# Performance work log

Hardware: AMD Instinct MI355X
Metric: run time of the kernel (lower is better)

Reference implementation:

```python
import jax, jax.numpy as jnp
import numpy as np

H = 64
V = 50257
B = 32
L = 4096
LN_EPS = 1e-5
DELTA_EPS = 1e-6


def setup_inputs() -> dict:
    key = jax.random.key(0)
    ks = jax.random.split(key, 10)
    s = 0.02
    return {
        "seq": jax.random.randint(ks[0], (B, L), 0, V),
        "read_pos": -1,
        "embed": jax.random.normal(ks[1], (V, H), jnp.float32) * s,
        "w1": jax.random.normal(ks[2], (H, 2 * H), jnp.float32) * s,
        "b1": jnp.zeros((2 * H,), jnp.float32),
        "w2": jax.random.normal(ks[3], (2 * H, H), jnp.float32) * s,
        "b2": jnp.zeros((H,), jnp.float32),
        "ln_g": jnp.ones((H,), jnp.float32),
        "ln_b": jnp.zeros((H,), jnp.float32),
        "rp_w": jax.random.normal(ks[4], (H, H), jnp.float32) * s,
        "rp_b": jnp.zeros((H,), jnp.float32),
        "out_w": jax.random.normal(ks[5], (H, V), jnp.float32) * s,
        "out_b": jnp.zeros((V,), jnp.float32),
    }


def _encoder(seq, embed, w1, b1, w2, b2, ln_g, ln_b):
    e = embed[seq]  # [B, L, H]
    f = jnp.maximum(e @ w1 + b1, 0.0) @ w2 + b2  # FFN
    x = e + f
    mu = jnp.mean(x, axis=-1, keepdims=True)
    var = jnp.mean((x - mu) ** 2, axis=-1, keepdims=True)
    return (x - mu) * jax.lax.rsqrt(var + LN_EPS) * ln_g + ln_b


def _delta_memory(h_all):
    # Strictly sequential delta-rule fast-weight update over t = 0..L-2.
    Bs, Ls, Hs = h_all.shape
    keys = jnp.transpose(h_all[:, : Ls - 1, :], (1, 0, 2))  # [L-1, B, H]

    def step(M, k):
        vp = jnp.einsum('bij,bj->bi', M, k)  # M @ k
        u = k - vp / (jnp.sum(k * k, axis=-1, keepdims=True) + DELTA_EPS)
        M = M + u[:, :, None] * k[:, None, :]  # outer product update
        return M, None

    M0 = jnp.zeros((Bs, Hs, Hs), h_all.dtype)
    M, _ = jax.lax.scan(step, M0, keys)
    return M


def reference(seq, read_pos, embed, w1, b1, w2, b2, ln_g, ln_b, rp_w, rp_b, out_w, out_b):
    h_all = _encoder(seq, embed, w1, b1, w2, b2, ln_g, ln_b)  # [B, L, H]
    M = _delta_memory(h_all)  # [B, H, H]
    q = h_all[:, read_pos, :]  # [B, H]
    r = jnp.einsum('bij,bj->bi', M, q)
    return (r @ rp_w + rp_b) @ out_w + out_b  # [B, V]
```

## Files before the change

kernel.cpp:

```cpp
#include <hip/hip_runtime.h>

#define HH 64
#define VV 50257
#define BB 32
#define LL 4096

constexpr float LN_EPS_F = 1e-5f;
constexpr float DELTA_EPS_F = 1e-6f;

constexpr int CS = 64;
constexpr int NG = LL / CS;

typedef float f32x4 __attribute__((ext_vector_type(4)));
typedef short bf16x8 __attribute__((ext_vector_type(8)));
union U16x8 { uint4 u; bf16x8 v; unsigned short s[8]; };

__device__ __forceinline__ unsigned short f2bf(float f) {
  union { float f; unsigned u; } v; v.f = f;
  unsigned r = v.u + 0x7fff + ((v.u >> 16) & 1);
  return (unsigned short)(r >> 16);
}

template <int CTRL>
__device__ __forceinline__ float dpp_add(float x) {
  int t = __builtin_amdgcn_update_dpp(0, __float_as_int(x), CTRL, 0xF, 0xF, true);
  return x + __int_as_float(t);
}

__device__ __forceinline__ float wave_sum_lane63(float x) {
  x = dpp_add<0x111>(x);
  x = dpp_add<0x112>(x);
  x = dpp_add<0x114>(x);
  x = dpp_add<0x118>(x);
  x = dpp_add<0x142>(x);
  x = dpp_add<0x143>(x);
  return x;
}

__device__ __forceinline__ float readlane_f(float x, int lane) {
  return __int_as_float(__builtin_amdgcn_readlane(__float_as_int(x), lane));
}

__global__ __launch_bounds__(256) void prep_kernel(
    const float* __restrict__ w1, const float* __restrict__ w2,
    unsigned short* __restrict__ w1b, unsigned short* __restrict__ w2b) {
  int i = blockIdx.x * 256 + threadIdx.x;
  if (i < 8192) {
    int jj = i >> 6, h = i & 63;
    w1b[i] = f2bf(w1[h * 128 + jj]);
  } else {
    int k = i - 8192;
    int h = k >> 7, jj = k & 127;
    w2b[k] = f2bf(w2[jj * 64 + h]);
  }
}

__global__ __launch_bounds__(64, 1) void encoder_kernel(
    const int* __restrict__ seq, const float* __restrict__ embed,
    const unsigned short* __restrict__ w1b, const float* __restrict__ b1,
    const unsigned short* __restrict__ w2b, const float* __restrict__ b2,
    const float* __restrict__ ln_g, const float* __restrict__ ln_b,
    float* __restrict__ h_all, float* __restrict__ beta) {
  __shared__ __align__(16) char pool[26624];
  unsigned short (*e_l)[72] = reinterpret_cast<unsigned short (*)[72]>(pool);
  unsigned short (*act_l)[136] = reinterpret_cast<unsigned short (*)[136]>(pool + 9216);
  float (*x_l)[65] = reinterpret_cast<float (*)[65]>(pool);
  __shared__ float2 gb_l[64];
  __shared__ float b1_l[128], b2_l[64];

  int lane = threadIdx.x;
  int q = lane >> 4, l = lane & 15;
  int base = blockIdx.x * 64;
  int s = seq[base + lane];

  {
    const float4* ep = reinterpret_cast<const float4*>(embed + (size_t)s * HH);
#pragma unroll
    for (int i = 0; i < 8; ++i) {
      float4 va = ep[2 * i], vb = ep[2 * i + 1];
      uint4 u;
      u.x = (unsigned)f2bf(va.x) | ((unsigned)f2bf(va.y) << 16);
      u.y = (unsigned)f2bf(va.z) | ((unsigned)f2bf(va.w) << 16);
      u.z = (unsigned)f2bf(vb.x) | ((unsigned)f2bf(vb.y) << 16);
      u.w = (unsigned)f2bf(vb.z) | ((unsigned)f2bf(vb.w) << 16);
      *(uint4*)&e_l[lane][8 * i] = u;
    }
  }
  gb_l[lane] = make_float2(ln_g[lane], ln_b[lane]);
  b1_l[lane] = b1[lane];
  b1_l[64 + lane] = b1[64 + lane];
  b2_l[lane] = b2[lane];

  bf16x8 af1[8][2];
#pragma unroll
  for (int mi = 0; mi < 8; ++mi)
#pragma unroll
    for (int ks = 0; ks < 2; ++ks) {
      U16x8 t;
      t.u = *(const uint4*)(w1b + (mi * 16 + l) * 64 + ks * 32 + q * 8);
      af1[mi][ks] = t.v;
    }

  __syncthreads();

  f32x4 acc1[8][4];
#pragma unroll
  for (int mi = 0; mi < 8; ++mi)
#pragma unroll
    for (int nt = 0; nt < 4; ++nt) acc1[mi][nt] = (f32x4){0.f, 0.f, 0.f, 0.f};

#pragma unroll
  for (int ks = 0; ks < 2; ++ks) {
    bf16x8 bfr[4];
#pragma unroll
    for (int nt = 0; nt < 4; ++nt) {
      U16x8 t;
      t.u = *(const uint4*)&e_l[nt * 16 + l][ks * 32 + q * 8];
      bfr[nt] = t.v;
    }
#pragma unroll
    for (int mi = 0; mi < 8; ++mi)
#pragma unroll
      for (int nt = 0; nt < 4; ++nt)
        acc1[mi][nt] = __builtin_amdgcn_mfma_f32_16x16x32_bf16(
            af1[mi][ks], bfr[nt], acc1[mi][nt], 0, 0, 0);
  }

#pragma unroll
  for (int mi = 0; mi < 8; ++mi)
#pragma unroll
    for (int nt = 0; nt < 4; ++nt) {
      int tok = nt * 16 + l;
      int jj0 = mi * 16 + q * 4;
      float v0 = fmaxf(acc1[mi][nt][0] + b1_l[jj0 + 0], 0.f);
      float v1 = fmaxf(acc1[mi][nt][1] + b1_l[jj0 + 1], 0.f);
      float v2 = fmaxf(acc1[mi][nt][2] + b1_l[jj0 + 2], 0.f);
      float v3 = fmaxf(acc1[mi][nt][3] + b1_l[jj0 + 3], 0.f);
      uint2 u;
      u.x = (unsigned)f2bf(v0) | ((unsigned)f2bf(v1) << 16);
      u.y = (unsigned)f2bf(v2) | ((unsigned)f2bf(v3) << 16);
      *(uint2*)&act_l[tok][jj0] = u;
    }

  bf16x8 bf2[4][4];
#pragma unroll
  for (int nt = 0; nt < 4; ++nt)
#pragma unroll
    for (int ks = 0; ks < 4; ++ks) {
      U16x8 t;
      t.u = *(const uint4*)(w2b + (nt * 16 + l) * 128 + ks * 32 + q * 8);
      bf2[nt][ks] = t.v;
    }

  __syncthreads();

  f32x4 acc2[4][4];
#pragma unroll
  for (int mt = 0; mt < 4; ++mt)
#pragma unroll
    for (int nt = 0; nt < 4; ++nt) acc2[mt][nt] = (f32x4){0.f, 0.f, 0.f, 0.f};

#pragma unroll
  for (int ks = 0; ks < 4; ++ks) {
    bf16x8 afr[4];
#pragma unroll
    for (int mt = 0; mt < 4; ++mt) {
      U16x8 t;
      t.u = *(const uint4*)&act_l[mt * 16 + l][ks * 32 + q * 8];
      afr[mt] = t.v;
    }
#pragma unroll
    for (int mt = 0; mt < 4; ++mt)
#pragma unroll
      for (int nt = 0; nt < 4; ++nt)
        acc2[mt][nt] = __builtin_amdgcn_mfma_f32_16x16x32_bf16(
            afr[mt], bf2[nt][ks], acc2[mt][nt], 0, 0, 0);
  }

  __syncthreads();

#pragma unroll
  for (int mt = 0; mt < 4; ++mt)
#pragma unroll
    for (int nt = 0; nt < 4; ++nt) {
      int h = nt * 16 + l;
#pragma unroll
      for (int r = 0; r < 4; ++r) {
        int tok = mt * 16 + q * 4 + r;
        x_l[tok][h] = acc2[mt][nt][r] + b2_l[h];
      }
    }

  __syncthreads();

  float x[HH];
#pragma unroll
  for (int h = 0; h < HH; ++h) x[h] = x_l[lane][h];
  {
    const float4* ep = reinterpret_cast<const float4*>(embed + (size_t)s * HH);
#pragma unroll
    for (int i = 0; i < 16; ++i) {
      float4 v = ep[i];
      x[4 * i + 0] += v.x; x[4 * i + 1] += v.y;
      x[4 * i + 2] += v.z; x[4 * i + 3] += v.w;
    }
  }
  float sum = 0.f;
#pragma unroll
  for (int h = 0; h < HH; ++h) sum += x[h];
  float mu = sum * (1.f / HH);
  float vs = 0.f;
#pragma unroll
  for (int h = 0; h < HH; ++h) { float dx = x[h] - mu; vs = fmaf(dx, dx, vs); }
  float rstd = rsqrtf(vs * (1.f / HH) + LN_EPS_F);

  float ss = 0.f;
#pragma unroll
  for (int h = 0; h < HH; ++h) {
    float2 gb = gb_l[h];
    float o = fmaf((x[h] - mu) * rstd, gb.x, gb.y);
    ss = fmaf(o, o, ss);
    x[h] = o;
  }
  float4* hp = reinterpret_cast<float4*>(h_all + (size_t)(base + lane) * HH);
#pragma unroll
  for (int i = 0; i < 16; ++i)
    hp[i] = make_float4(x[4 * i + 0], x[4 * i + 1], x[4 * i + 2], x[4 * i + 3]);
  beta[base + lane] = 1.f / (ss + DELTA_EPS_F);
}

__global__ __launch_bounds__(64, 1) void gram_n_kernel(
    const float* __restrict__ h_all, const float* __restrict__ beta,
    float* __restrict__ Ng) {
  __shared__ __align__(16) char smem[37120];
  unsigned short (*pA)[64][72] = reinterpret_cast<unsigned short (*)[64][72]>(smem);
  unsigned short (*pB)[64][72] = reinterpret_cast<unsigned short (*)[64][72]>(smem + 18432);
  float* Glp = reinterpret_cast<float*>(smem + 18432);
  float* bl = reinterpret_cast<float*>(smem + 36864);

  int c = blockIdx.x, b = blockIdx.y, lane = threadIdx.x;
  int q = lane >> 4, l = lane & 15;
  const float* src = h_all + ((size_t)b * LL + c * CS) * HH;

  bf16x8 ah[2][4], al_[2][4];
#pragma unroll
  for (int ks = 0; ks < 2; ++ks)
#pragma unroll
    for (int i = 0; i < 4; ++i) {
      const float* p = src + (i * 16 + l) * 64 + ks * 32 + q * 8;
      float4 va = *(const float4*)p, vb = *(const float4*)(p + 4);
      float f[8] = {va.x, va.y, va.z, va.w, vb.x, vb.y, vb.z, vb.w};
      U16x8 hi, lo;
#pragma unroll
      for (int r = 0; r < 8; ++r) {
        unsigned short hb = f2bf(f[r]);
        hi.s[r] = hb;
        lo.s[r] = f2bf(f[r] - __uint_as_float(((unsigned)hb) << 16));
      }
      ah[ks][i] = hi.v; al_[ks][i] = lo.v;
    }
  if (c == NG - 1 && l == 15) {
#pragma unroll
    for (int ks = 0; ks < 2; ++ks) {
      ah[ks][3] = (bf16x8){0, 0, 0, 0, 0, 0, 0, 0};
      al_[ks][3] = (bf16x8){0, 0, 0, 0, 0, 0, 0, 0};
    }
  }

  bl[lane] = beta[(size_t)b * LL + c * CS + lane];

  float m[64];
#pragma unroll
  for (int t = 0; t < 64; ++t) m[t] = src[t * 64 + lane];
  if (c == NG - 1) m[63] = 0.f;

  f32x4 acc[4][4];
#pragma unroll
  for (int mi = 0; mi < 4; ++mi)
#pragma unroll
    for (int nt = 0; nt <= mi; ++nt) acc[mi][nt] = (f32x4){0.f, 0.f, 0.f, 0.f};

#pragma unroll
  for (int ks = 0; ks < 2; ++ks)
#pragma unroll
    for (int mi = 0; mi < 4; ++mi)
#pragma unroll
      for (int nt = 0; nt <= mi; ++nt) {
        acc[mi][nt] = __builtin_amdgcn_mfma_f32_16x16x32_bf16(ah[ks][mi], ah[ks][nt], acc[mi][nt], 0, 0, 0);
        acc[mi][nt] = __builtin_amdgcn_mfma_f32_16x16x32_bf16(ah[ks][mi], al_[ks][nt], acc[mi][nt], 0, 0, 0);
        acc[mi][nt] = __builtin_amdgcn_mfma_f32_16x16x32_bf16(al_[ks][mi], ah[ks][nt], acc[mi][nt], 0, 0, 0);
      }

#pragma unroll
  for (int mi = 0; mi < 4; ++mi) {
    int gg = 4 * mi + q;
    int e1 = 8 * gg * (gg + 1);
    int o0 = 4 * gg * (2 * gg + 1);
    int o1 = e1;
    int o2 = e1 + 4 * (gg + 1);
    int o3 = e1 + 8 * (gg + 1);
#pragma unroll
    for (int nt = 0; nt < mi; ++nt) {
      int t = nt * 16 + l;
      Glp[o0 + t] = acc[mi][nt][0];
      Glp[o1 + t] = acc[mi][nt][1];
      Glp[o2 + t] = acc[mi][nt][2];
      Glp[o3 + t] = acc[mi][nt][3];
    }
    {
      int t = mi * 16 + l;
      if (l < 4 * q)     Glp[o0 + t] = acc[mi][mi][0];
      if (l < 4 * q + 1) Glp[o1 + t] = acc[mi][mi][1];
      if (l < 4 * q + 2) Glp[o2 + t] = acc[mi][mi][2];
      if (l < 4 * q + 3) Glp[o3 + t] = acc[mi][mi][3];
    }
  }

#pragma unroll
  for (int i = 0; i < 16; ++i) {
    float v0 = m[4 * i], v1 = m[4 * i + 1], v2 = m[4 * i + 2], v3 = m[4 * i + 3];
    unsigned short h0 = f2bf(v0), h1 = f2bf(v1), h2 = f2bf(v2), h3 = f2bf(v3);
    float r0 = v0 - __uint_as_float(((unsigned)h0) << 16);
    float r1 = v1 - __uint_as_float(((unsigned)h1) << 16);
    float r2 = v2 - __uint_as_float(((unsigned)h2) << 16);
    float r3 = v3 - __uint_as_float(((unsigned)h3) << 16);
    *(uint2*)&pA[0][lane][4 * i] = make_uint2(
        (unsigned)h0 | (((unsigned)h1) << 16), (unsigned)h2 | (((unsigned)h3) << 16));
    *(uint2*)&pA[1][lane][4 * i] = make_uint2(
        (unsigned)f2bf(r0) | (((unsigned)f2bf(r1)) << 16),
        (unsigned)f2bf(r2) | (((unsigned)f2bf(r3)) << 16));
  }
  __syncthreads();

#pragma unroll
  for (int g = 15; g >= 0; --g) {
    int e1 = 8 * g * (g + 1);
    int o0 = 4 * g * (2 * g + 1);
    int o1 = e1;
    int o2 = e1 + 4 * (g + 1);
    int o3 = e1 + 8 * (g + 1);
    float4 C1 = *(const float4*)(Glp + o1 + 4 * g);
    float4 C2 = *(const float4*)(Glp + o2 + 4 * g);
    float4 C3 = *(const float4*)(Glp + o3 + 4 * g);
    float4 B4 = *(const float4*)(bl + 4 * g);

    float t3 = B4.w * m[4 * g + 3];
    float v2 = fmaf(-C3.z, t3, m[4 * g + 2]);
    float t2 = B4.z * v2;
    float v1 = fmaf(-C2.y, t2, fmaf(-C3.y, t3, m[4 * g + 1]));
    float t1 = B4.y * v1;
    float v0 = fmaf(-C1.x, t1, fmaf(-C2.x, t2, fmaf(-C3.x, t3, m[4 * g + 0])));
    float t0 = B4.x * v0;
    m[4 * g + 0] = t0; m[4 * g + 1] = t1; m[4 * g + 2] = t2; m[4 * g + 3] = t3;

#pragma unroll
    for (int j = 0; j < g; ++j) {
      float4 R0 = *(const float4*)(Glp + o0 + 4 * j);
      float4 R1 = *(const float4*)(Glp + o1 + 4 * j);
      float4 R2 = *(const float4*)(Glp + o2 + 4 * j);
      float4 R3 = *(const float4*)(Glp + o3 + 4 * j);
      m[4 * j + 0] = fmaf(-R3.x, t3, fmaf(-R2.x, t2, fmaf(-R1.x, t1, fmaf(-R0.x, t0, m[4 * j + 0]))));
      m[4 * j + 1] = fmaf(-R3.y, t3, fmaf(-R2.y, t2, fmaf(-R1.y, t1, fmaf(-R0.y, t0, m[4 * j + 1]))));
      m[4 * j + 2] = fmaf(-R3.z, t3, fmaf(-R2.z, t2, fmaf(-R1.z, t1, fmaf(-R0.z, t0, m[4 * j + 2]))));
      m[4 * j + 3] = fmaf(-R3.w, t3, fmaf(-R2.w, t2, fmaf(-R1.w, t1, fmaf(-R0.w, t0, m[4 * j + 3]))));
    }
  }

  __syncthreads();

#pragma unroll
  for (int i = 0; i < 16; ++i) {
    float v0 = m[4 * i], v1 = m[4 * i + 1], v2 = m[4 * i + 2], v3 = m[4 * i + 3];
    unsigned short h0 = f2bf(v0), h1 = f2bf(v1), h2 = f2bf(v2), h3 = f2bf(v3);
    float r0 = v0 - __uint_as_float(((unsigned)h0) << 16);
    float r1 = v1 - __uint_as_float(((unsigned)h1) << 16);
    float r2 = v2 - __uint_as_float(((unsigned)h2) << 16);
    float r3 = v3 - __uint_as_float(((unsigned)h3) << 16);
    *(uint2*)&pB[0][lane][4 * i] = make_uint2(
        (unsigned)h0 | (((unsigned)h1) << 16), (unsigned)h2 | (((unsigned)h3) << 16));
    *(uint2*)&pB[1][lane][4 * i] = make_uint2(
        (unsigned)f2bf(r0) | (((unsigned)f2bf(r1)) << 16),
        (unsigned)f2bf(r2) | (((unsigned)f2bf(r3)) << 16));
  }
  __syncthreads();

  f32x4 acc2[4][4];
#pragma unroll
  for (int mi = 0; mi < 4; ++mi)
#pragma unroll
    for (int nt = 0; nt < 4; ++nt) acc2[mi][nt] = (f32x4){0.f, 0.f, 0.f, 0.f};

#pragma unroll
  for (int ks = 0; ks < 2; ++ks) {
    bf16x8 kh[4], kl_[4], bh[4], blo[4];
#pragma unroll
    for (int i = 0; i < 4; ++i) {
      U16x8 t;
      t.u = *(const uint4*)&pA[0][i * 16 + l][ks * 32 + q * 8]; kh[i] = t.v;
      t.u = *(const uint4*)&pA[1][i * 16 + l][ks * 32 + q * 8]; kl_[i] = t.v;
      t.u = *(const uint4*)&pB[0][i * 16 + l][ks * 32 + q * 8]; bh[i] = t.v;
      t.u = *(const uint4*)&pB[1][i * 16 + l][ks * 32 + q * 8]; blo[i] = t.v;
    }
#pragma unroll
    for (int mi = 0; mi < 4; ++mi)
#pragma unroll
      for (int nt = 0; nt < 4; ++nt) {
        acc2[mi][nt] = __builtin_amdgcn_mfma_f32_16x16x32_bf16(kh[mi], bh[nt], acc2[mi][nt], 0, 0, 0);
        acc2[mi][nt] = __builtin_amdgcn_mfma_f32_16x16x32_bf16(kh[mi], blo[nt], acc2[mi][nt], 0, 0, 0);
        acc2[mi][nt] = __builtin_amdgcn_mfma_f32_16x16x32_bf16(kl_[mi], bh[nt], acc2[mi][nt], 0, 0, 0);
      }
  }

  float* np = Ng + (((size_t)b * NG + c) << 12);
#pragma unroll
  for (int mi = 0; mi < 4; ++mi)
#pragma unroll
    for (int nt = 0; nt < 4; ++nt) {
      int h0 = mi * 16 + q * 4, hp = nt * 16 + l;
      float4 v;
      v.x = ((h0 + 0 == hp) ? 1.f : 0.f) - acc2[mi][nt][0];
      v.y = ((h0 + 1 == hp) ? 1.f : 0.f) - acc2[mi][nt][1];
      v.z = ((h0 + 2 == hp) ? 1.f : 0.f) - acc2[mi][nt][2];
      v.w = ((h0 + 3 == hp) ? 1.f : 0.f) - acc2[mi][nt][3];
      *(float4*)&np[hp * 64 + h0] = v;
    }
}

__global__ __launch_bounds__(64, 1) void boundary_kernel(
    const float* __restrict__ h_all, const float* __restrict__ Ng,
    const int* __restrict__ read_pos_p, float* __restrict__ Qg) {
  __shared__ __align__(16) float nt0[64 * 64];
  __shared__ __align__(16) float nt1[64 * 64];
  __shared__ __align__(16) float ql[64];

  int b = blockIdx.x, lane = threadIdx.x;
  int rpv = read_pos_p[0];
  int pos = rpv < 0 ? rpv + LL : rpv;
  float Q = h_all[((size_t)b * LL + pos) * HH + lane];

  const float* Nb = Ng + ((size_t)b * NG << 12);

  auto load_chunk = [&](float* buf, int c) {
    const float* g = Nb + ((size_t)c << 12);
#pragma unroll
    for (int i = 0; i < 16; ++i)
      __builtin_amdgcn_global_load_lds(
          (const __attribute__((address_space(1))) unsigned*)(g + i * 256 + lane * 4),
          (__attribute__((address_space(3))) unsigned*)(buf + i * 256), 16, 0, 0);
  };

  auto step = [&](const float* buf, int c, bool last) {
    if (last) __builtin_amdgcn_s_waitcnt(0x0F70);
    else      __builtin_amdgcn_s_waitcnt(0x4F70);
    Qg[((size_t)b * NG + c) * HH + lane] = Q;
    ql[lane] = Q;
    float a0 = 0.f, a1 = 0.f, a2 = 0.f, a3 = 0.f;
#pragma unroll
    for (int j = 0; j < 64; j += 4) {
      float4 q4 = *(const float4*)&ql[j];
      a0 = fmaf(buf[(j + 0) * 64 + lane], q4.x, a0);
      a1 = fmaf(buf[(j + 1) * 64 + lane], q4.y, a1);
      a2 = fmaf(buf[(j + 2) * 64 + lane], q4.z, a2);
      a3 = fmaf(buf[(j + 3) * 64 + lane], q4.w, a3);
    }
    Q = (a0 + a1) + (a2 + a3);
  };

  load_chunk(nt1, NG - 1);
  load_chunk(nt0, NG - 2);

#pragma unroll 1
  for (int c = NG - 1; c >= 1; c -= 2) {
    step(nt1, c, false);
    __builtin_amdgcn_s_waitcnt(0xC07F);
    if (c >= 3) load_chunk(nt1, c - 2);
    step(nt0, c - 1, c == 1);
    __builtin_amdgcn_s_waitcnt(0xC07F);
    if (c >= 3) load_chunk(nt0, c - 3);
  }
}

__global__ __launch_bounds__(64, 1) void chunk_scan_kernel(
    const float* __restrict__ h_all, const float* __restrict__ beta,
    const float* __restrict__ Qg, float* __restrict__ rc) {
  int c = blockIdx.x, b = blockIdx.y, j = threadIdx.x;
  const float* hb = h_all + (size_t)b * LL * HH;
  const float* betab = beta + (size_t)b * LL;

  float P = Qg[((size_t)b * NG + c) * HH + j];
  float r = 0.f;

  float kk[CS];
#pragma unroll
  for (int i = 0; i < CS; ++i) kk[i] = hb[((size_t)(c * CS + i)) * HH + j];
  float bv = betab[c * CS + j];

  bool last = (c == NG - 1);
#pragma unroll
  for (int i = CS - 1; i >= 0; --i) {
    float k = kk[i];
    float bt = readlane_f(bv, i);
    float m = k * P;
    float s = wave_sum_lane63(m);
    float d = readlane_f(s, 63);
    if (i == CS - 1 && last) d = 0.f;
    r = fmaf(d, k, r);
    P = fmaf(-(bt * d), k, P);
  }
  rc[((size_t)b * NG + c) * HH + j] = r;
}

__global__ __launch_bounds__(64, 1) void combine_kernel(
    const float* __restrict__ rc, const float* __restrict__ rp_w,
    const float* __restrict__ rp_b, float* __restrict__ yv) {
  int b = blockIdx.x, j = threadIdx.x;
  float r = 0.f;
#pragma unroll 8
  for (int cc = 0; cc < NG; ++cc) r += rc[((size_t)b * NG + cc) * HH + j];
  __shared__ float rs[HH];
  rs[j] = r;
  __syncthreads();
  float yj = rp_b[j];
#pragma unroll
  for (int h = 0; h < HH; ++h) yj = fmaf(rs[h], rp_w[h * HH + j], yj);
  yv[b * HH + j] = yj;
}

__global__ __launch_bounds__(256, 2) void out_kernel(
    const float* __restrict__ yv, const float* __restrict__ out_w,
    const float* __restrict__ out_b, float* __restrict__ out) {
  __shared__ float ys[BB * HH];
  for (int i = threadIdx.x; i < BB * HH; i += 256) ys[i] = yv[i];
  __syncthreads();

  int v = blockIdx.x * 256 + threadIdx.x;
  if (v >= VV) return;

  float acc[BB];
  float ob = out_b[v];
#pragma unroll
  for (int b = 0; b < BB; ++b) acc[b] = ob;

  for (int h = 0; h < HH; ++h) {
    float w = out_w[(size_t)h * VV + v];
#pragma unroll
    for (int b = 0; b < BB; ++b) acc[b] = fmaf(ys[b * HH + h], w, acc[b]);
  }
#pragma unroll
  for (int b = 0; b < BB; ++b) out[(size_t)b * VV + v] = acc[b];
}

extern "C" void kernel_launch(void* const* d_in, const int* in_sizes, int n_in,
                              void* d_out, int out_size, void* d_ws, size_t ws_size,
                              hipStream_t stream) {
  (void)in_sizes; (void)n_in; (void)out_size; (void)ws_size;
  const int*   seq   = (const int*)d_in[0];
  const int*   rp    = (const int*)d_in[1];
  const float* embed = (const float*)d_in[2];
  const float* w1    = (const float*)d_in[3];
  const float* b1    = (const float*)d_in[4];
  const float* w2    = (const float*)d_in[5];
  const float* b2    = (const float*)d_in[6];
  const float* ln_g  = (const float*)d_in[7];
  const float* ln_b  = (const float*)d_in[8];
  const float* rp_w  = (const float*)d_in[9];
  const float* rp_b  = (const float*)d_in[10];
  const float* out_w = (const float*)d_in[11];
  const float* out_b = (const float*)d_in[12];
  float* out = (float*)d_out;

  float* h_all = (float*)d_ws;
  float* beta  = h_all + (size_t)BB * LL * HH;
  float* Ng    = beta + (size_t)BB * LL;
  float* Qg    = Ng + (size_t)BB * NG * HH * HH;
  float* rcv   = Qg + (size_t)BB * NG * HH;
  float* yv    = rcv + (size_t)BB * NG * HH;
  unsigned short* w1b = (unsigned short*)(yv + (size_t)BB * HH);
  unsigned short* w2b = w1b + 8192;

  prep_kernel<<<64, 256, 0, stream>>>(w1, w2, w1b, w2b);
  encoder_kernel<<<BB * LL / 64, 64, 0, stream>>>(seq, embed, w1b, b1, w2b, b2,
                                                  ln_g, ln_b, h_all, beta);
  gram_n_kernel<<<dim3(NG, BB), 64, 0, stream>>>(h_all, beta, Ng);
  boundary_kernel<<<BB, 64, 0, stream>>>(h_all, Ng, rp, Qg);
  chunk_scan_kernel<<<dim3(NG, BB), 64, 0, stream>>>(h_all, beta, Qg, rcv);
  combine_kernel<<<BB, 64, 0, stream>>>(rcv, rp_w, rp_b, yv);
  out_kernel<<<(VV + 255) / 256, 256, 0, stream>>>(yv, out_w, out_b, out);
}
```

Before: 232.1 us.

## Use packed bf16 conversion, packed FMA solve, and half-staged swizzled LDS

Replaces the software bf16 rounding with the hardware v_cvt_pk_bf16_f32 instruction in the encoder and the gram kernel. The triangular-solve state becomes float2 vectors so the inner updates can use packed FMA. The pB staging buffer is cut to two XOR-swizzled half buffers that are filled per k-step, which shrinks the gram kernel's LDS from about 37KB to about 27KB and avoids bank conflicts. The cost is extra __syncthreads inside the k loop, and the hardware conversion's rounding may differ slightly from the manual round-to-nearest-even.

After: 235.3 us. Within noise of the previous version (+1.4%).

```diff
diff --git a/kernel.cpp b/kernel.cpp
--- a/kernel.cpp
+++ b/kernel.cpp
@@ -12,6 +12,7 @@
 constexpr int NG = LL / CS;
 
 typedef float f32x4 __attribute__((ext_vector_type(4)));
+typedef float f32x2 __attribute__((ext_vector_type(2)));
 typedef short bf16x8 __attribute__((ext_vector_type(8)));
 union U16x8 { uint4 u; bf16x8 v; unsigned short s[8]; };
 
@@ -19,6 +20,19 @@
   union { float f; unsigned u; } v; v.f = f;
   unsigned r = v.u + 0x7fff + ((v.u >> 16) & 1);
   return (unsigned short)(r >> 16);
+}
+
+__device__ __forceinline__ unsigned cvt_pk_bf16(float a, float b) {
+  unsigned r;
+  asm("v_cvt_pk_bf16_f32 %0, %1, %2" : "=v"(r) : "v"(a), "v"(b));
+  return r;
+}
+
+__device__ __forceinline__ void split2(float a, float b, unsigned& hp, unsigned& lp) {
+  hp = cvt_pk_bf16(a, b);
+  float ha = __uint_as_float(hp << 16);
+  float hb = __uint_as_float(hp & 0xffff0000u);
+  lp = cvt_pk_bf16(a - ha, b - hb);
 }
 
 template <int CTRL>
@@ -79,10 +93,10 @@
     for (int i = 0; i < 8; ++i) {
       float4 va = ep[2 * i], vb = ep[2 * i + 1];
       uint4 u;
-      u.x = (unsigned)f2bf(va.x) | ((unsigned)f2bf(va.y) << 16);
-      u.y = (unsigned)f2bf(va.z) | ((unsigned)f2bf(va.w) << 16);
-      u.z = (unsigned)f2bf(vb.x) | ((unsigned)f2bf(vb.y) << 16);
-      u.w = (unsigned)f2bf(vb.z) | ((unsigned)f2bf(vb.w) << 16);
+      u.x = cvt_pk_bf16(va.x, va.y);
+      u.y = cvt_pk_bf16(va.z, va.w);
+      u.z = cvt_pk_bf16(vb.x, vb.y);
+      u.w = cvt_pk_bf16(vb.z, vb.w);
       *(uint4*)&e_l[lane][8 * i] = u;
     }
   }
@@ -137,8 +151,8 @@
       float v2 = fmaxf(acc1[mi][nt][2] + b1_l[jj0 + 2], 0.f);
       float v3 = fmaxf(acc1[mi][nt][3] + b1_l[jj0 + 3], 0.f);
       uint2 u;
-      u.x = (unsigned)f2bf(v0) | ((unsigned)f2bf(v1) << 16);
-      u.y = (unsigned)f2bf(v2) | ((unsigned)f2bf(v3) << 16);
+      u.x = cvt_pk_bf16(v0, v1);
+      u.y = cvt_pk_bf16(v2, v3);
       *(uint2*)&act_l[tok][jj0] = u;
     }
 
@@ -232,11 +246,11 @@
 __global__ __launch_bounds__(64, 1) void gram_n_kernel(
     const float* __restrict__ h_all, const float* __restrict__ beta,
     float* __restrict__ Ng) {
-  __shared__ __align__(16) char smem[37120];
+  __shared__ __align__(16) char smem[27136];
   unsigned short (*pA)[64][72] = reinterpret_cast<unsigned short (*)[64][72]>(smem);
-  unsigned short (*pB)[64][72] = reinterpret_cast<unsigned short (*)[64][72]>(smem + 18432);
   float* Glp = reinterpret_cast<float*>(smem + 18432);
-  float* bl = reinterpret_cast<float*>(smem + 36864);
+  char* pBh0 = smem + 18432;
+  float* bl = reinterpret_cast<float*>(smem + 26880);
 
   int c = blockIdx.x, b = blockIdx.y, lane = threadIdx.x;
   int q = lane >> 4, l = lane & 15;
@@ -249,14 +263,11 @@
     for (int i = 0; i < 4; ++i) {
       const float* p = src + (i * 16 + l) * 64 + ks * 32 + q * 8;
       float4 va = *(const float4*)p, vb = *(const float4*)(p + 4);
-      float f[8] = {va.x, va.y, va.z, va.w, vb.x, vb.y, vb.z, vb.w};
       U16x8 hi, lo;
-#pragma unroll
-      for (int r = 0; r < 8; ++r) {
-        unsigned short hb = f2bf(f[r]);
-        hi.s[r] = hb;
-        lo.s[r] = f2bf(f[r] - __uint_as_float(((unsigned)hb) << 16));
-      }
+      split2(va.x, va.y, hi.u.x, lo.u.x);
+      split2(va.z, va.w, hi.u.y, lo.u.y);
+      split2(vb.x, vb.y, hi.u.z, lo.u.z);
+      split2(vb.z, vb.w, hi.u.w, lo.u.w);
       ah[ks][i] = hi.v; al_[ks][i] = lo.v;
     }
   if (c == NG - 1 && l == 15) {
@@ -269,10 +280,11 @@
 
   bl[lane] = beta[(size_t)b * LL + c * CS + lane];
 
-  float m[64];
-#pragma unroll
-  for (int t = 0; t < 64; ++t) m[t] = src[t * 64 + lane];
-  if (c == NG - 1) m[63] = 0.f;
+  f32x2 m2[32];
+#pragma unroll
+  for (int t = 0; t < 32; ++t)
+    m2[t] = (f32x2){src[(2 * t) * 64 + lane], src[(2 * t + 1) * 64 + lane]};
+  if (c == NG - 1) m2[31].y = 0.f;
 
   f32x4 acc[4][4];
 #pragma unroll
@@ -318,17 +330,11 @@
 
 #pragma unroll
   for (int i = 0; i < 16; ++i) {
-    float v0 = m[4 * i], v1 = m[4 * i + 1], v2 = m[4 * i + 2], v3 = m[4 * i + 3];
-    unsigned short h0 = f2bf(v0), h1 = f2bf(v1), h2 = f2bf(v2), h3 = f2bf(v3);
-    float r0 = v0 - __uint_as_float(((unsigned)h0) << 16);
-    float r1 = v1 - __uint_as_float(((unsigned)h1) << 16);
-    float r2 = v2 - __uint_as_float(((unsigned)h2) << 16);
-    float r3 = v3 - __uint_as_float(((unsigned)h3) << 16);
-    *(uint2*)&pA[0][lane][4 * i] = make_uint2(
-        (unsigned)h0 | (((unsigned)h1) << 16), (unsigned)h2 | (((unsigned)h3) << 16));
-    *(uint2*)&pA[1][lane][4 * i] = make_uint2(
-        (unsigned)f2bf(r0) | (((unsigned)f2bf(r1)) << 16),
-        (unsigned)f2bf(r2) | (((unsigned)f2bf(r3)) << 16));
+    unsigned h0, l0, h1, l1;
+    split2(m2[2 * i].x, m2[2 * i].y, h0, l0);
+    split2(m2[2 * i + 1].x, m2[2 * i + 1].y, h1, l1);
+    *(uint2*)&pA[0][lane][4 * i] = make_uint2(h0, h1);
+    *(uint2*)&pA[1][lane][4 * i] = make_uint2(l0, l1);
   }
   __syncthreads();
 
@@ -344,14 +350,16 @@
     float4 C3 = *(const float4*)(Glp + o3 + 4 * g);
     float4 B4 = *(const float4*)(bl + 4 * g);
 
-    float t3 = B4.w * m[4 * g + 3];
-    float v2 = fmaf(-C3.z, t3, m[4 * g + 2]);
+    float t3 = B4.w * m2[2 * g + 1].y;
+    float v2 = fmaf(-C3.z, t3, m2[2 * g + 1].x);
     float t2 = B4.z * v2;
-    float v1 = fmaf(-C2.y, t2, fmaf(-C3.y, t3, m[4 * g + 1]));
+    float v1 = fmaf(-C2.y, t2, fmaf(-C3.y, t3, m2[2 * g].y));
     float t1 = B4.y * v1;
-    float v0 = fmaf(-C1.x, t1, fmaf(-C2.x, t2, fmaf(-C3.x, t3, m[4 * g + 0])));
+    float v0 = fmaf(-C1.x, t1, fmaf(-C2.x, t2, fmaf(-C3.x, t3, m2[2 * g].x)));
     float t0 = B4.x * v0;
-    m[4 * g + 0] = t0; m[4 * g + 1] = t1; m[4 * g + 2] = t2; m[4 * g + 3] = t3;
+    m2[2 * g] = (f32x2){t0, t1};
+    m2[2 * g + 1] = (f32x2){t2, t3};
+    f32x2 n0 = {-t0, -t0}, n1 = {-t1, -t1}, n2 = {-t2, -t2}, n3 = {-t3, -t3};
 
 #pragma unroll
     for (int j = 0; j < g; ++j) {
@@ -359,29 +367,19 @@
       float4 R1 = *(const float4*)(Glp + o1 + 4 * j);
       float4 R2 = *(const float4*)(Glp + o2 + 4 * j);
       float4 R3 = *(const float4*)(Glp + o3 + 4 * j);
-      m[4 * j + 0] = fmaf(-R3.x, t3, fmaf(-R2.x, t2, fmaf(-R1.x, t1, fmaf(-R0.x, t0, m[4 * j + 0]))));
-      m[4 * j + 1] = fmaf(-R3.y, t3, fmaf(-R2.y, t2, fmaf(-R1.y, t1, fmaf(-R0.y, t0, m[4 * j + 1]))));
-      m[4 * j + 2] = fmaf(-R3.z, t3, fmaf(-R2.z, t2, fmaf(-R1.z, t1, fmaf(-R0.z, t0, m[4 * j + 2]))));
-      m[4 * j + 3] = fmaf(-R3.w, t3, fmaf(-R2.w, t2, fmaf(-R1.w, t1, fmaf(-R0.w, t0, m[4 * j + 3]))));
-    }
-  }
-
-  __syncthreads();
-
-#pragma unroll
-  for (int i = 0; i < 16; ++i) {
-    float v0 = m[4 * i], v1 = m[4 * i + 1], v2 = m[4 * i + 2], v3 = m[4 * i + 3];
-    unsigned short h0 = f2bf(v0), h1 = f2bf(v1), h2 = f2bf(v2), h3 = f2bf(v3);
-    float r0 = v0 - __uint_as_float(((unsigned)h0) << 16);
-    float r1 = v1 - __uint_as_float(((unsigned)h1) << 16);
-    float r2 = v2 - __uint_as_float(((unsigned)h2) << 16);
-    float r3 = v3 - __uint_as_float(((unsigned)h3) << 16);
-    *(uint2*)&pB[0][lane][4 * i] = make_uint2(
-        (unsigned)h0 | (((unsigned)h1) << 16), (unsigned)h2 | (((unsigned)h3) << 16));
-    *(uint2*)&pB[1][lane][4 * i] = make_uint2(
-        (unsigned)f2bf(r0) | (((unsigned)f2bf(r1)) << 16),
-        (unsigned)f2bf(r2) | (((unsigned)f2bf(r3)) << 16));
-  }
+      f32x2 a = m2[2 * j], d = m2[2 * j + 1];
+      a = __builtin_elementwise_fma((f32x2){R0.x, R0.y}, n0, a);
+      a = __builtin_elementwise_fma((f32x2){R1.x, R1.y}, n1, a);
+      a = __builtin_elementwise_fma((f32x2){R2.x, R2.y}, n2, a);
+      a = __builtin_elementwise_fma((f32x2){R3.x, R3.y}, n3, a);
+      d = __builtin_elementwise_fma((f32x2){R0.z, R0.w}, n0, d);
+      d = __builtin_elementwise_fma((f32x2){R1.z, R1.w}, n1, d);
+      d = __builtin_elementwise_fma((f32x2){R2.z, R2.w}, n2, d);
+      d = __builtin_elementwise_fma((f32x2){R3.z, R3.w}, n3, d);
+      m2[2 * j] = a; m2[2 * j + 1] = d;
+    }
+  }
+
   __syncthreads();
 
   f32x4 acc2[4][4];
@@ -391,15 +389,28 @@
     for (int nt = 0; nt < 4; ++nt) acc2[mi][nt] = (f32x4){0.f, 0.f, 0.f, 0.f};
 
 #pragma unroll
-  for (int ks = 0; ks < 2; ++ks) {
+  for (int hf = 0; hf < 2; ++hf) {
+#pragma unroll
+    for (int i2 = 0; i2 < 8; ++i2) {
+      int tt = hf * 16 + 2 * i2;
+      unsigned h0, l0, h1, l1;
+      split2(m2[tt].x, m2[tt].y, h0, l0);
+      split2(m2[tt + 1].x, m2[tt + 1].y, h1, l1);
+      unsigned boff = (unsigned)((lane * 64 + i2 * 8) ^ ((lane & 7) << 4));
+      *(uint2*)(pBh0 + boff) = make_uint2(h0, h1);
+      *(uint2*)(pBh0 + 4096 + boff) = make_uint2(l0, l1);
+    }
+    __syncthreads();
+
     bf16x8 kh[4], kl_[4], bh[4], blo[4];
 #pragma unroll
     for (int i = 0; i < 4; ++i) {
       U16x8 t;
-      t.u = *(const uint4*)&pA[0][i * 16 + l][ks * 32 + q * 8]; kh[i] = t.v;
-      t.u = *(const uint4*)&pA[1][i * 16 + l][ks * 32 + q * 8]; kl_[i] = t.v;
-      t.u = *(const uint4*)&pB[0][i * 16 + l][ks * 32 + q * 8]; bh[i] = t.v;
-      t.u = *(const uint4*)&pB[1][i * 16 + l][ks * 32 + q * 8]; blo[i] = t.v;
+      t.u = *(const uint4*)&pA[0][i * 16 + l][hf * 32 + q * 8]; kh[i] = t.v;
+      t.u = *(const uint4*)&pA[1][i * 16 + l][hf * 32 + q * 8]; kl_[i] = t.v;
+      unsigned bro = (unsigned)((((16 * i + l) * 64) + q * 16) ^ ((l & 7) << 4));
+      t.u = *(const uint4*)(pBh0 + bro);        bh[i] = t.v;
+      t.u = *(const uint4*)(pBh0 + 4096 + bro); blo[i] = t.v;
     }
 #pragma unroll
     for (int mi = 0; mi < 4; ++mi)
@@ -409,6 +420,7 @@
         acc2[mi][nt] = __builtin_amdgcn_mfma_f32_16x16x32_bf16(kh[mi], blo[nt], acc2[mi][nt], 0, 0, 0);
         acc2[mi][nt] = __builtin_amdgcn_mfma_f32_16x16x32_bf16(kl_[mi], bh[nt], acc2[mi][nt], 0, 0, 0);
       }
+    __syncthreads();
   }
 
   float* np = Ng + (((size_t)b * NG + c) << 12);
```
